# Kernel optimization log

Hardware: AMD Instinct MI355X
Metric: run time of the kernel (lower is better)

The kernel has to match this reference:

```python
import jax, jax.numpy as jnp
import numpy as np

B, D, T = 8, 1024, 512
HID, NH, NL = 256, 4, 2
OUT = HID // NH  # 64 per-head dim
ALPHA = 0.2      # leaky relu slope
EPS = 1e-5       # layernorm eps


def setup_inputs() -> dict:
    key = jax.random.key(0)
    ks = jax.random.split(key, 10)
    X_obs = jax.random.normal(ks[0], (B, D, T), dtype=jnp.float32)
    mask = (jax.random.uniform(ks[1], (B, D, T)) < 0.8).astype(jnp.float32)
    W_in = jax.random.normal(ks[2], (2 * T, HID), dtype=jnp.float32) * (1.0 / np.sqrt(2 * T))
    b_in = jnp.zeros((HID,), dtype=jnp.float32)
    gat_W = jax.random.normal(ks[3], (NL, NH, HID, OUT), dtype=jnp.float32) * (1.0 / np.sqrt(HID))
    gat_a = jax.random.normal(ks[4], (NL, NH, 2 * OUT), dtype=jnp.float32) * 0.1
    ln_g = jnp.ones((NL, HID), dtype=jnp.float32)
    ln_b = jnp.zeros((NL, HID), dtype=jnp.float32)
    W_out = jax.random.normal(ks[5], (HID, T), dtype=jnp.float32) * (1.0 / np.sqrt(HID))
    b_out = jnp.zeros((T,), dtype=jnp.float32)
    return dict(X_obs=X_obs, mask=mask, W_in=W_in, b_in=b_in, gat_W=gat_W,
                gat_a=gat_a, ln_g=ln_g, ln_b=ln_b, W_out=W_out, b_out=b_out)


def _layer_norm(x, g, b):
    mu = jnp.mean(x, axis=-1, keepdims=True)
    var = jnp.mean((x - mu) ** 2, axis=-1, keepdims=True)
    return (x - mu) * jax.lax.rsqrt(var + EPS) * g + b


def _gat_forward(X_obs, mask, W_in, b_in, gat_W, gat_a, ln_g, ln_b, W_out, b_out):
    # mean-impute per (d, t) position across batch
    obs_sum = jnp.sum(X_obs * mask, axis=0, keepdims=True)
    obs_cnt = jnp.sum(mask, axis=0, keepdims=True)
    pos_mean = obs_sum / (obs_cnt + 1e-10)
    X_mean = X_obs * mask + (1.0 - mask) * pos_mean

    x = jnp.concatenate([X_mean, mask], axis=-1)       # (B, D, 2T)
    h = x @ W_in + b_in                                 # (B, N, HID)

    for l in range(NL):
        Wl = gat_W[l]                                   # (H, HID, OUT)
        a_left = gat_a[l, :, :OUT]                      # (H, OUT)
        a_right = gat_a[l, :, OUT:]                     # (H, OUT)
        hW = jnp.einsum('bnd,hde->bhne', h, Wl)         # (B, H, N, OUT)
        # e_ij = leakyrelu(a_left . h_i + a_right . h_j) -- avoids O(N^2 * 2d) concat
        s_l = jnp.einsum('bhne,he->bhn', hW, a_left)
        s_r = jnp.einsum('bhne,he->bhn', hW, a_right)
        e = jax.nn.leaky_relu(s_l[..., :, None] + s_r[..., None, :], ALPHA)  # (B,H,N,N)
        attn = jax.nn.softmax(e, axis=-1)
        head_out = jnp.einsum('bhnm,bhme->bhne', attn, hW)                   # (B,H,N,OUT)
        h_new = jnp.transpose(head_out, (0, 2, 1, 3)).reshape(h.shape[0], h.shape[1], HID)
        h = _layer_norm(h + h_new, ln_g[l], ln_b[l])

    return h @ W_out + b_out                            # (B, D, T)


def reference(X_obs, mask, W_in, b_in, gat_W, gat_a, ln_g, ln_b, W_out, b_out):
    return _gat_forward(X_obs, mask, W_in, b_in, gat_W, gat_a, ln_g, ln_b, W_out, b_out)
```

## Files before the change

kernel.cpp:

```cpp
#include <hip/hip_runtime.h>
#include <hip/hip_bf16.h>

constexpr int B_   = 8;
constexpr int D_   = 1024;
constexpr int T_   = 512;
constexpr int HID_ = 256;
constexpr int NH_  = 4;
constexpr int NL_  = 2;
constexpr float ALPHA_ = 0.2f;
constexpr float EPS_   = 1e-5f;
constexpr int OUT_ = 64;
constexpr int M_ = B_ * D_;
constexpr int DT_ = D_ * T_;
constexpr int KIN_ = 2 * T_;

typedef __attribute__((ext_vector_type(8))) short short8;
typedef __attribute__((ext_vector_type(4))) float floatx4;

__device__ __forceinline__ unsigned short f2bf(float f) {
    unsigned int u = __float_as_uint(f);
    unsigned int r = u + 0x7fffu + ((u >> 16) & 1u);
    return (unsigned short)(r >> 16);
}
__device__ __forceinline__ unsigned int kenc(float f) {
    unsigned int u = __float_as_uint(f);
    return (u & 0x80000000u) ? ~u : (u | 0x80000000u);
}
__device__ __forceinline__ float kdec(unsigned int k) {
    unsigned int u = (k & 0x80000000u) ? (k ^ 0x80000000u) : ~k;
    return __uint_as_float(u);
}

__global__ __launch_bounds__(256) void prep_k(const float* __restrict__ X,
                                              const float* __restrict__ Mk,
                                              const float* __restrict__ W_in,
                                              const float* __restrict__ gatW,
                                              const float* __restrict__ W_out,
                                              unsigned short* __restrict__ Ain,
                                              unsigned short* __restrict__ Wt_in,
                                              unsigned short* __restrict__ Wcat,
                                              unsigned short* __restrict__ WtO,
                                              unsigned int* __restrict__ rmaxkey) {
    int bx = blockIdx.x;
    if (bx < 512) {
        int idx4 = (bx * 256 + threadIdx.x) * 4;
        int t = idx4 & (T_ - 1);
        int d = idx4 >> 9;
        float4 x[B_], m[B_];
        float4 s = {0, 0, 0, 0}, c = {0, 0, 0, 0};
#pragma unroll
        for (int b = 0; b < B_; b++) {
            x[b] = *(const float4*)&X[(size_t)b * DT_ + idx4];
            m[b] = *(const float4*)&Mk[(size_t)b * DT_ + idx4];
            s.x += x[b].x * m[b].x; s.y += x[b].y * m[b].y;
            s.z += x[b].z * m[b].z; s.w += x[b].w * m[b].w;
            c.x += m[b].x; c.y += m[b].y; c.z += m[b].z; c.w += m[b].w;
        }
        float4 pm;
        pm.x = s.x / (c.x + 1e-10f); pm.y = s.y / (c.y + 1e-10f);
        pm.z = s.z / (c.z + 1e-10f); pm.w = s.w / (c.w + 1e-10f);
#pragma unroll
        for (int b = 0; b < B_; b++) {
            size_t row = (size_t)b * D_ + d;
            ushort4 xm, mk;
            xm.x = f2bf(x[b].x * m[b].x + (1.f - m[b].x) * pm.x);
            xm.y = f2bf(x[b].y * m[b].y + (1.f - m[b].y) * pm.y);
            xm.z = f2bf(x[b].z * m[b].z + (1.f - m[b].z) * pm.z);
            xm.w = f2bf(x[b].w * m[b].w + (1.f - m[b].w) * pm.w);
            mk.x = f2bf(m[b].x); mk.y = f2bf(m[b].y);
            mk.z = f2bf(m[b].z); mk.w = f2bf(m[b].w);
            *(ushort4*)&Ain[row * KIN_ + t]      = xm;
            *(ushort4*)&Ain[row * KIN_ + T_ + t] = mk;
        }
    } else {
        int idx = (bx - 512) * 256 + threadIdx.x;
        if (idx < 64) rmaxkey[idx] = 0u;
        if (idx < 262144) {
            int n = idx >> 10, k = idx & 1023;
            Wt_in[idx] = f2bf(W_in[(size_t)k * HID_ + n]);
        } else if (idx < 393216) {
            int j = idx - 262144;
            int l = j >> 16, n = (j >> 8) & 255, k = j & 255;
            int h = n >> 6, e = n & 63;
            Wcat[j] = f2bf(gatW[(((size_t)(l * NH_ + h) * HID_) + k) * OUT_ + e]);
        } else {
            int j = idx - 393216;
            int n = j >> 8, k = j & 255;
            WtO[j] = f2bf(W_out[(size_t)k * T_ + n]);
        }
    }
}

template <int MODE>
__global__ __launch_bounds__(256) void gemm_bf16_k(
        const unsigned short* __restrict__ A,
        const unsigned short* __restrict__ Bt,
        const float* __restrict__ bias,
        float* __restrict__ C,
        unsigned short* __restrict__ Cb,
        const float* __restrict__ ga,
        float* __restrict__ s_l,
        float* __restrict__ s_r,
        unsigned int* __restrict__ rmaxkey,
        int Nsz, int Ksz) {
    __shared__ __align__(16) unsigned short As[2][64 * 72];
    __shared__ __align__(16) unsigned short Bs[2][64 * 72];
    int tid = threadIdx.x;
    int wave = tid >> 6, lane = tid & 63;
    int q = lane >> 4, r16 = lane & 15;
    int rowbase = blockIdx.y * 64;
    int colbase = blockIdx.x * 64;

    int srow = tid >> 3, sk = (tid & 7) * 8;
    const unsigned short* Ap0 = A + (size_t)(rowbase + srow) * Ksz + sk;
    const unsigned short* Ap1 = A + (size_t)(rowbase + srow + 32) * Ksz + sk;
    const unsigned short* Bp0 = Bt + (size_t)(colbase + srow) * Ksz + sk;
    const unsigned short* Bp1 = Bt + (size_t)(colbase + srow + 32) * Ksz + sk;
    int la0 = srow * 72 + sk, la1 = (srow + 32) * 72 + sk;

    floatx4 acc[4];
#pragma unroll
    for (int i = 0; i < 4; i++) acc[i] = (floatx4)0.f;

    uint4 pa0 = *(const uint4*)Ap0, pa1 = *(const uint4*)Ap1;
    uint4 pb0 = *(const uint4*)Bp0, pb1 = *(const uint4*)Bp1;
    *(uint4*)&As[0][la0] = pa0;
    *(uint4*)&As[0][la1] = pa1;
    *(uint4*)&Bs[0][la0] = pb0;
    *(uint4*)&Bs[0][la1] = pb1;

    int nk = Ksz >> 6;
    for (int it = 0; it < nk; it++) {
        int cur = it & 1;
        __syncthreads();
        if (it + 1 < nk) {
            int kt = (it + 1) << 6;
            pa0 = *(const uint4*)(Ap0 + kt);
            pa1 = *(const uint4*)(Ap1 + kt);
            pb0 = *(const uint4*)(Bp0 + kt);
            pb1 = *(const uint4*)(Bp1 + kt);
        }
#pragma unroll
        for (int t = 0; t < 2; t++) {
            short8 a = *(const short8*)&As[cur][(wave * 16 + r16) * 72 + t * 32 + q * 8];
#pragma unroll
            for (int ni = 0; ni < 4; ni++) {
                short8 b = *(const short8*)&Bs[cur][(ni * 16 + r16) * 72 + t * 32 + q * 8];
                acc[ni] = __builtin_amdgcn_mfma_f32_16x16x32_bf16(a, b, acc[ni], 0, 0, 0);
            }
        }
        if (it + 1 < nk) {
            int nxt = cur ^ 1;
            *(uint4*)&As[nxt][la0] = pa0;
            *(uint4*)&As[nxt][la1] = pa1;
            *(uint4*)&Bs[nxt][la0] = pb0;
            *(uint4*)&Bs[nxt][la1] = pb1;
        }
    }
    if constexpr (MODE == 2) {
        int bhh = ((rowbase >> 10) << 2) + blockIdx.x;
        int nb = (rowbase & (D_ - 1)) + wave * 16;
#pragma unroll
        for (int ni = 0; ni < 4; ni++) {
            int e = ni * 16 + r16;
            ushort4 pk;
            pk.x = f2bf(acc[ni][0]);
            pk.y = f2bf(acc[ni][1]);
            pk.z = f2bf(acc[ni][2]);
            pk.w = f2bf(acc[ni][3]);
            *(ushort4*)&Cb[((size_t)(bhh * 64 + e) << 10) + nb + q * 4] = pk;
        }
        const float* gab = ga + blockIdx.x * 2 * OUT_;
        float al4[4], ar4[4];
#pragma unroll
        for (int ni = 0; ni < 4; ni++) {
            al4[ni] = gab[ni * 16 + r16];
            ar4[ni] = gab[OUT_ + ni * 16 + r16];
        }
        float slv[4], srv[4];
#pragma unroll
        for (int rr = 0; rr < 4; rr++) {
            float s1 = 0.f, s2 = 0.f;
#pragma unroll
            for (int ni = 0; ni < 4; ni++) {
                s1 += acc[ni][rr] * al4[ni];
                s2 += acc[ni][rr] * ar4[ni];
            }
            slv[rr] = s1;
            srv[rr] = s2;
        }
#pragma unroll
        for (int off = 1; off < 16; off <<= 1) {
#pragma unroll
            for (int rr = 0; rr < 4; rr++) {
                slv[rr] += __shfl_xor(slv[rr], off, 64);
                srv[rr] += __shfl_xor(srv[rr], off, 64);
            }
        }
        {
            int rsel = r16 & 3;
            float sv = (rsel == 0) ? slv[0] : (rsel == 1) ? slv[1] : (rsel == 2) ? slv[2] : slv[3];
            float rv = (rsel == 0) ? srv[0] : (rsel == 1) ? srv[1] : (rsel == 2) ? srv[2] : srv[3];
            int n = nb + q * 4 + rsel;
            if (r16 < 4)                 s_l[bhh * D_ + n] = sv;
            else if (r16 >= 8 && r16 < 12) s_r[bhh * D_ + n] = rv;
        }
        float mx = fmaxf(fmaxf(srv[0], srv[1]), fmaxf(srv[2], srv[3]));
        mx = fmaxf(mx, __shfl_xor(mx, 16, 64));
        mx = fmaxf(mx, __shfl_xor(mx, 32, 64));
        if (lane == 0) atomicMax(&rmaxkey[bhh], kenc(mx));
    } else {
#pragma unroll
        for (int rr = 0; rr < 4; rr++) {
            int row = rowbase + wave * 16 + q * 4 + rr;
#pragma unroll
            for (int ni = 0; ni < 4; ni++) {
                int col = colbase + ni * 16 + r16;
                float v = acc[ni][rr] + (bias ? bias[col] : 0.f);
                C[(size_t)row * Nsz + col] = v;
                if constexpr (MODE == 1) Cb[(size_t)row * Nsz + col] = f2bf(v);
            }
        }
    }
}

__global__ __launch_bounds__(256) void attn_k(const unsigned short* __restrict__ hwT,
                                              const float* __restrict__ sl_g,
                                              const float* __restrict__ sr_g,
                                              const unsigned int* __restrict__ rmaxkey,
                                              float* __restrict__ pacc,
                                              float* __restrict__ pden) {
    int bh = blockIdx.x;
    int b = bh >> 2, h = bh & 3;
    int half = blockIdx.z;
    int mb = half * 512;
    int tid = threadIdx.x;
    int wave = tid >> 6, lane = tid & 63;
    int q = lane >> 4, r16 = lane & 15;

    __shared__ float srs[512];
    __shared__ __align__(16) unsigned short Vt[2][64][136];

    *(float2*)&srs[tid * 2] = *(const float2*)&sr_g[bh * D_ + mb + tid * 2];

    float rm = kdec(rmaxkey[bh]);
    int row0 = blockIdx.y * 64 + wave * 16;
    float sl = sl_g[bh * D_ + row0 + r16];
    float xm = sl + rm;
    float Mn = fmaxf(xm, ALPHA_ * xm);

    floatx4 acc[4];
#pragma unroll
    for (int i = 0; i < 4; i++) acc[i] = (floatx4)0.f;
    float dsum = 0.f;

    const unsigned short* vbase = hwT + ((size_t)(bh * 64) << 10) + mb;
    int se[4], sp[4];
#pragma unroll
    for (int i = 0; i < 4; i++) {
        int s = tid + i * 256;
        se[i] = s >> 4;
        sp[i] = (s & 15) * 8;
    }

    uint4 pre[4];
#pragma unroll
    for (int i = 0; i < 4; i++)
        pre[i] = *(const uint4*)&vbase[((size_t)se[i] << 10) + sp[i]];
#pragma unroll
    for (int i = 0; i < 4; i++)
        *(uint4*)&Vt[0][se[i]][sp[i]] = pre[i];
    __syncthreads();

    for (int c = 0; c < 4; c++) {
        int cur = c & 1;
        if (c < 3) {
            int mo = (c + 1) * 128;
#pragma unroll
            for (int i = 0; i < 4; i++)
                pre[i] = *(const uint4*)&vbase[((size_t)se[i] << 10) + mo + sp[i]];
        }
#pragma unroll
        for (int kk = 0; kk < 128; kk += 32) {
            int m0 = c * 128 + kk + q * 8;
            float4 s0 = *(const float4*)&srs[m0];
            float4 s1 = *(const float4*)&srs[m0 + 4];
            float sr8[8] = {s0.x, s0.y, s0.z, s0.w, s1.x, s1.y, s1.z, s1.w};
            float p[8];
#pragma unroll
            for (int j = 0; j < 8; j++) {
                float x = sl + sr8[j];
                float e = fmaxf(x, ALPHA_ * x);
                float pj = __expf(e - Mn);
                dsum += pj;
                p[j] = pj;
            }
            union { unsigned int u[4]; short8 s8; } cv;
#pragma unroll
            for (int j = 0; j < 4; j++) {
                unsigned int lo = (__float_as_uint(p[2 * j]) + 0x8000u) >> 16;
                unsigned int hi = (__float_as_uint(p[2 * j + 1]) + 0x8000u) & 0xffff0000u;
                cv.u[j] = hi | lo;
            }
#pragma unroll
            for (int ni = 0; ni < 4; ni++) {
                short8 bfr = *(const short8*)&Vt[cur][ni * 16 + r16][kk + q * 8];
                acc[ni] = __builtin_amdgcn_mfma_f32_16x16x32_bf16(cv.s8, bfr, acc[ni], 0, 0, 0);
            }
        }
        if (c < 3) {
#pragma unroll
            for (int i = 0; i < 4; i++)
                *(uint4*)&Vt[cur ^ 1][se[i]][sp[i]] = pre[i];
        }
        __syncthreads();
    }
    dsum += __shfl_xor(dsum, 16);
    dsum += __shfl_xor(dsum, 32);
    size_t gr0 = (size_t)b * D_ + row0;
    if (lane < 16) pden[((size_t)half * M_ + gr0 + r16) * NH_ + h] = dsum;
#pragma unroll
    for (int rr = 0; rr < 4; rr++) {
        size_t grow = gr0 + q * 4 + rr;
#pragma unroll
        for (int ni = 0; ni < 4; ni++) {
            pacc[((size_t)half * M_ + grow) * HID_ + h * OUT_ + ni * 16 + r16] = acc[ni][rr];
        }
    }
}

__global__ __launch_bounds__(256) void addln_k(float* __restrict__ h,
                                               const float* __restrict__ pacc,
                                               const float* __restrict__ pden,
                                               const float* __restrict__ g,
                                               const float* __restrict__ bb,
                                               unsigned short* __restrict__ hbf) {
    int wave = threadIdx.x >> 6, lane = threadIdx.x & 63;
    size_t row = (size_t)blockIdx.x * 4 + wave;
    float4 a  = *(const float4*)&h[row * HID_ + lane * 4];
    float4 p0 = *(const float4*)&pacc[row * HID_ + lane * 4];
    float4 p1 = *(const float4*)&pacc[((size_t)M_ + row) * HID_ + lane * 4];
    int hh = lane >> 4;
    float den = pden[row * NH_ + hh] + pden[((size_t)M_ + row) * NH_ + hh];
    float inv = 1.f / den;
    float4 v = {a.x + (p0.x + p1.x) * inv, a.y + (p0.y + p1.y) * inv,
                a.z + (p0.z + p1.z) * inv, a.w + (p0.w + p1.w) * inv};
    float s = v.x + v.y + v.z + v.w;
#pragma unroll
    for (int off = 1; off < 64; off <<= 1) s += __shfl_xor(s, off, 64);
    float mu = s * (1.f / HID_);
    float4 d = {v.x - mu, v.y - mu, v.z - mu, v.w - mu};
    float s2 = d.x * d.x + d.y * d.y + d.z * d.z + d.w * d.w;
#pragma unroll
    for (int off = 1; off < 64; off <<= 1) s2 += __shfl_xor(s2, off, 64);
    float rs = rsqrtf(s2 * (1.f / HID_) + EPS_);
    float4 gg = *(const float4*)&g[lane * 4];
    float4 bbv = *(const float4*)&bb[lane * 4];
    float4 res;
    res.x = d.x * rs * gg.x + bbv.x;
    res.y = d.y * rs * gg.y + bbv.y;
    res.z = d.z * rs * gg.z + bbv.z;
    res.w = d.w * rs * gg.w + bbv.w;
    *(float4*)&h[row * HID_ + lane * 4] = res;
    ushort4 pk = {f2bf(res.x), f2bf(res.y), f2bf(res.z), f2bf(res.w)};
    *(ushort4*)&hbf[row * HID_ + lane * 4] = pk;
}

extern "C" void kernel_launch(void* const* d_in, const int* in_sizes, int n_in,
                              void* d_out, int out_size, void* d_ws, size_t ws_size,
                              hipStream_t stream) {
    const float* X_obs = (const float*)d_in[0];
    const float* mask  = (const float*)d_in[1];
    const float* W_in  = (const float*)d_in[2];
    const float* b_in  = (const float*)d_in[3];
    const float* gat_W = (const float*)d_in[4];
    const float* gat_a = (const float*)d_in[5];
    const float* ln_g  = (const float*)d_in[6];
    const float* ln_b  = (const float*)d_in[7];
    const float* W_out = (const float*)d_in[8];
    const float* b_out = (const float*)d_in[9];
    float* out = (float*)d_out;

    char* base = (char*)d_ws;
    unsigned short* Ain  = (unsigned short*)base;
    unsigned short* hwT  = (unsigned short*)base;
    float* pacc = (float*)(base + (4u << 20));
    float* pden = (float*)(base + (20u << 20));
    float* hbuf = (float*)(base + (21u << 20));
    unsigned short* hbf   = (unsigned short*)(base + (29u << 20));
    unsigned short* Wt_in = (unsigned short*)(base + (33u << 20));
    unsigned short* Wcat  = Wt_in + (size_t)HID_ * KIN_;
    unsigned short* WtO   = Wcat + (size_t)NL_ * HID_ * HID_;
    float* slb = (float*)(WtO + (size_t)T_ * HID_);
    float* srb = slb + B_ * NH_ * D_;
    unsigned int* rmaxkey = (unsigned int*)(srb + B_ * NH_ * D_);

    prep_k<<<2560, 256, 0, stream>>>(X_obs, mask, W_in, gat_W, W_out,
                                     Ain, Wt_in, Wcat, WtO, rmaxkey);

    gemm_bf16_k<1><<<dim3(HID_ / 64, M_ / 64), 256, 0, stream>>>(
        Ain, Wt_in, b_in, hbuf, hbf, nullptr, nullptr, nullptr, nullptr,
        HID_, KIN_);

    for (int l = 0; l < NL_; l++) {
        gemm_bf16_k<2><<<dim3(HID_ / 64, M_ / 64), 256, 0, stream>>>(
            hbf, Wcat + (size_t)l * HID_ * HID_, nullptr, nullptr, hwT,
            gat_a + (size_t)l * NH_ * 2 * OUT_, slb, srb, rmaxkey + l * 32,
            HID_, HID_);
        attn_k<<<dim3(B_ * NH_, D_ / 64, 2), 256, 0, stream>>>(
            hwT, slb, srb, rmaxkey + l * 32, pacc, pden);
        addln_k<<<M_ / 4, 256, 0, stream>>>(hbuf, pacc, pden,
                                            ln_g + (size_t)l * HID_,
                                            ln_b + (size_t)l * HID_, hbf);
    }

    gemm_bf16_k<0><<<dim3(T_ / 64, M_ / 64), 256, 0, stream>>>(
        hbf, WtO, b_out, out, nullptr, nullptr, nullptr, nullptr, nullptr,
        T_, HID_);
}
```

Before: 217.0 us.

## Fuse residual layernorm into following GEMM and drop attention key-split

The separate add+layernorm kernel is removed. Its work is now done in a prologue of the next projection GEMM, which normalizes its 64-row A tile in shared memory. The attention kernel no longer splits the key dimension into two halves: each block walks all 1024 keys and writes normalized head outputs directly, so the partial accumulator and denominator buffers go away. In exchange, the layernorm is recomputed by every column block of the GEMM (4 or 8 times), and the attention grid halves, giving fewer blocks to fill the GPU.

```diff
diff --git a/kernel.cpp b/kernel.cpp
--- a/kernel.cpp
+++ b/kernel.cpp
@@ -228,20 +228,17 @@
                                               const float* __restrict__ sl_g,
                                               const float* __restrict__ sr_g,
                                               const unsigned int* __restrict__ rmaxkey,
-                                              float* __restrict__ pacc,
-                                              float* __restrict__ pden) {
+                                              float* __restrict__ hnew) {
     int bh = blockIdx.x;
     int b = bh >> 2, h = bh & 3;
-    int half = blockIdx.z;
-    int mb = half * 512;
     int tid = threadIdx.x;
     int wave = tid >> 6, lane = tid & 63;
     int q = lane >> 4, r16 = lane & 15;
 
-    __shared__ float srs[512];
+    __shared__ float srs[1024];
     __shared__ __align__(16) unsigned short Vt[2][64][136];
 
-    *(float2*)&srs[tid * 2] = *(const float2*)&sr_g[bh * D_ + mb + tid * 2];
+    *(float4*)&srs[tid * 4] = *(const float4*)&sr_g[bh * D_ + tid * 4];
 
     float rm = kdec(rmaxkey[bh]);
     int row0 = blockIdx.y * 64 + wave * 16;
@@ -254,7 +251,7 @@
     for (int i = 0; i < 4; i++) acc[i] = (floatx4)0.f;
     float dsum = 0.f;
 
-    const unsigned short* vbase = hwT + ((size_t)(bh * 64) << 10) + mb;
+    const unsigned short* vbase = hwT + ((size_t)(bh * 64) << 10);
     int se[4], sp[4];
 #pragma unroll
     for (int i = 0; i < 4; i++) {
@@ -272,9 +269,9 @@
         *(uint4*)&Vt[0][se[i]][sp[i]] = pre[i];
     __syncthreads();
 
-    for (int c = 0; c < 4; c++) {
+    for (int c = 0; c < 8; c++) {
         int cur = c & 1;
-        if (c < 3) {
+        if (c < 7) {
             int mo = (c + 1) * 128;
 #pragma unroll
             for (int i = 0; i < 4; i++)
@@ -308,7 +305,7 @@
                 acc[ni] = __builtin_amdgcn_mfma_f32_16x16x32_bf16(cv.s8, bfr, acc[ni], 0, 0, 0);
             }
         }
-        if (c < 3) {
+        if (c < 7) {
 #pragma unroll
             for (int i = 0; i < 4; i++)
                 *(uint4*)&Vt[cur ^ 1][se[i]][sp[i]] = pre[i];
@@ -317,53 +314,168 @@
     }
     dsum += __shfl_xor(dsum, 16);
     dsum += __shfl_xor(dsum, 32);
-    size_t gr0 = (size_t)b * D_ + row0;
-    if (lane < 16) pden[((size_t)half * M_ + gr0 + r16) * NH_ + h] = dsum;
 #pragma unroll
     for (int rr = 0; rr < 4; rr++) {
-        size_t grow = gr0 + q * 4 + rr;
+        float inv = 1.f / __shfl(dsum, q * 4 + rr, 64);
+        size_t off = ((size_t)(b * D_ + row0 + q * 4 + rr)) * HID_ + h * OUT_;
+#pragma unroll
+        for (int ni = 0; ni < 4; ni++)
+            hnew[off + ni * 16 + r16] = acc[ni][rr] * inv;
+    }
+}
+
+template <int MODE>
+__global__ __launch_bounds__(256) void gemmln_k(
+        const float* __restrict__ hbase,
+        const float* __restrict__ hnewIn,
+        const float* __restrict__ lng,
+        const float* __restrict__ lnb,
+        float* __restrict__ hout,
+        const unsigned short* __restrict__ Bt,
+        const float* __restrict__ bias,
+        float* __restrict__ C,
+        unsigned short* __restrict__ Cb,
+        const float* __restrict__ ga,
+        float* __restrict__ s_l,
+        float* __restrict__ s_r,
+        unsigned int* __restrict__ rmaxkey,
+        int Nsz) {
+    __shared__ __align__(16) unsigned short Asf[64 * 264];
+    __shared__ __align__(16) unsigned short Bs[2][64 * 72];
+    int tid = threadIdx.x;
+    int wave = tid >> 6, lane = tid & 63;
+    int q = lane >> 4, r16 = lane & 15;
+    int rowbase = blockIdx.y * 64;
+    int colbase = blockIdx.x * 64;
+
+    {
+        float4 gg = *(const float4*)&lng[lane * 4];
+        float4 bv = *(const float4*)&lnb[lane * 4];
+        for (int rr = 0; rr < 16; ++rr) {
+            int row = wave * 16 + rr;
+            size_t grow = (size_t)(rowbase + row) * HID_ + lane * 4;
+            float4 a  = *(const float4*)&hbase[grow];
+            float4 nv = *(const float4*)&hnewIn[grow];
+            float4 v = {a.x + nv.x, a.y + nv.y, a.z + nv.z, a.w + nv.w};
+            float s = v.x + v.y + v.z + v.w;
+#pragma unroll
+            for (int off = 1; off < 64; off <<= 1) s += __shfl_xor(s, off, 64);
+            float mu = s * (1.f / HID_);
+            float4 dd = {v.x - mu, v.y - mu, v.z - mu, v.w - mu};
+            float s2 = dd.x * dd.x + dd.y * dd.y + dd.z * dd.z + dd.w * dd.w;
+#pragma unroll
+            for (int off = 1; off < 64; off <<= 1) s2 += __shfl_xor(s2, off, 64);
+            float rs = rsqrtf(s2 * (1.f / HID_) + EPS_);
+            float4 res;
+            res.x = dd.x * rs * gg.x + bv.x;
+            res.y = dd.y * rs * gg.y + bv.y;
+            res.z = dd.z * rs * gg.z + bv.z;
+            res.w = dd.w * rs * gg.w + bv.w;
+            if (hout && blockIdx.x == 0) *(float4*)&hout[grow] = res;
+            ushort4 pk = {f2bf(res.x), f2bf(res.y), f2bf(res.z), f2bf(res.w)};
+            *(ushort4*)&Asf[row * 264 + lane * 4] = pk;
+        }
+    }
+    int srow = tid >> 3, sk = (tid & 7) * 8;
+    const unsigned short* Bp0 = Bt + (size_t)(colbase + srow) * HID_ + sk;
+    const unsigned short* Bp1 = Bt + (size_t)(colbase + srow + 32) * HID_ + sk;
+    int la0 = srow * 72 + sk, la1 = (srow + 32) * 72 + sk;
+    uint4 pb0 = *(const uint4*)Bp0, pb1 = *(const uint4*)Bp1;
+    *(uint4*)&Bs[0][la0] = pb0;
+    *(uint4*)&Bs[0][la1] = pb1;
+    __syncthreads();
+
+    floatx4 acc[4];
+#pragma unroll
+    for (int i = 0; i < 4; i++) acc[i] = (floatx4)0.f;
+
+    constexpr int nk = HID_ / 64;
+    for (int it = 0; it < nk; it++) {
+        int cur = it & 1;
+        if (it + 1 < nk) {
+            int kt = (it + 1) << 6;
+            pb0 = *(const uint4*)(Bp0 + kt);
+            pb1 = *(const uint4*)(Bp1 + kt);
+        }
+#pragma unroll
+        for (int t = 0; t < 2; t++) {
+            short8 a = *(const short8*)&Asf[(wave * 16 + r16) * 264 + it * 64 + t * 32 + q * 8];
+#pragma unroll
+            for (int ni = 0; ni < 4; ni++) {
+                short8 b = *(const short8*)&Bs[cur][(ni * 16 + r16) * 72 + t * 32 + q * 8];
+                acc[ni] = __builtin_amdgcn_mfma_f32_16x16x32_bf16(a, b, acc[ni], 0, 0, 0);
+            }
+        }
+        if (it + 1 < nk) {
+            int nxt = cur ^ 1;
+            *(uint4*)&Bs[nxt][la0] = pb0;
+            *(uint4*)&Bs[nxt][la1] = pb1;
+        }
+        __syncthreads();
+    }
+    if constexpr (MODE == 2) {
+        int bhh = ((rowbase >> 10) << 2) + blockIdx.x;
+        int nb = (rowbase & (D_ - 1)) + wave * 16;
 #pragma unroll
         for (int ni = 0; ni < 4; ni++) {
-            pacc[((size_t)half * M_ + grow) * HID_ + h * OUT_ + ni * 16 + r16] = acc[ni][rr];
-        }
-    }
-}
-
-__global__ __launch_bounds__(256) void addln_k(float* __restrict__ h,
-                                               const float* __restrict__ pacc,
-                                               const float* __restrict__ pden,
-                                               const float* __restrict__ g,
-                                               const float* __restrict__ bb,
-                                               unsigned short* __restrict__ hbf) {
-    int wave = threadIdx.x >> 6, lane = threadIdx.x & 63;
-    size_t row = (size_t)blockIdx.x * 4 + wave;
-    float4 a  = *(const float4*)&h[row * HID_ + lane * 4];
-    float4 p0 = *(const float4*)&pacc[row * HID_ + lane * 4];
-    float4 p1 = *(const float4*)&pacc[((size_t)M_ + row) * HID_ + lane * 4];
-    int hh = lane >> 4;
-    float den = pden[row * NH_ + hh] + pden[((size_t)M_ + row) * NH_ + hh];
-    float inv = 1.f / den;
-    float4 v = {a.x + (p0.x + p1.x) * inv, a.y + (p0.y + p1.y) * inv,
-                a.z + (p0.z + p1.z) * inv, a.w + (p0.w + p1.w) * inv};
-    float s = v.x + v.y + v.z + v.w;
-#pragma unroll
-    for (int off = 1; off < 64; off <<= 1) s += __shfl_xor(s, off, 64);
-    float mu = s * (1.f / HID_);
-    float4 d = {v.x - mu, v.y - mu, v.z - mu, v.w - mu};
-    float s2 = d.x * d.x + d.y * d.y + d.z * d.z + d.w * d.w;
-#pragma unroll
-    for (int off = 1; off < 64; off <<= 1) s2 += __shfl_xor(s2, off, 64);
-    float rs = rsqrtf(s2 * (1.f / HID_) + EPS_);
-    float4 gg = *(const float4*)&g[lane * 4];
-    float4 bbv = *(const float4*)&bb[lane * 4];
-    float4 res;
-    res.x = d.x * rs * gg.x + bbv.x;
-    res.y = d.y * rs * gg.y + bbv.y;
-    res.z = d.z * rs * gg.z + bbv.z;
-    res.w = d.w * rs * gg.w + bbv.w;
-    *(float4*)&h[row * HID_ + lane * 4] = res;
-    ushort4 pk = {f2bf(res.x), f2bf(res.y), f2bf(res.z), f2bf(res.w)};
-    *(ushort4*)&hbf[row * HID_ + lane * 4] = pk;
+            int e = ni * 16 + r16;
+            ushort4 pk;
+            pk.x = f2bf(acc[ni][0]);
+            pk.y = f2bf(acc[ni][1]);
+            pk.z = f2bf(acc[ni][2]);
+            pk.w = f2bf(acc[ni][3]);
+            *(ushort4*)&Cb[((size_t)(bhh * 64 + e) << 10) + nb + q * 4] = pk;
+        }
+        const float* gab = ga + blockIdx.x * 2 * OUT_;
+        float al4[4], ar4[4];
+#pragma unroll
+        for (int ni = 0; ni < 4; ni++) {
+            al4[ni] = gab[ni * 16 + r16];
+            ar4[ni] = gab[OUT_ + ni * 16 + r16];
+        }
+        float slv[4], srv[4];
+#pragma unroll
+        for (int rr = 0; rr < 4; rr++) {
+            float s1 = 0.f, s2 = 0.f;
+#pragma unroll
+            for (int ni = 0; ni < 4; ni++) {
+                s1 += acc[ni][rr] * al4[ni];
+                s2 += acc[ni][rr] * ar4[ni];
+            }
+            slv[rr] = s1;
+            srv[rr] = s2;
+        }
+#pragma unroll
+        for (int off = 1; off < 16; off <<= 1) {
+#pragma unroll
+            for (int rr = 0; rr < 4; rr++) {
+                slv[rr] += __shfl_xor(slv[rr], off, 64);
+                srv[rr] += __shfl_xor(srv[rr], off, 64);
+            }
+        }
+        {
+            int rsel = r16 & 3;
+            float sv = (rsel == 0) ? slv[0] : (rsel == 1) ? slv[1] : (rsel == 2) ? slv[2] : slv[3];
+            float rv = (rsel == 0) ? srv[0] : (rsel == 1) ? srv[1] : (rsel == 2) ? srv[2] : srv[3];
+            int n = nb + q * 4 + rsel;
+            if (r16 < 4)                 s_l[bhh * D_ + n] = sv;
+            else if (r16 >= 8 && r16 < 12) s_r[bhh * D_ + n] = rv;
+        }
+        float mx = fmaxf(fmaxf(srv[0], srv[1]), fmaxf(srv[2], srv[3]));
+        mx = fmaxf(mx, __shfl_xor(mx, 16, 64));
+        mx = fmaxf(mx, __shfl_xor(mx, 32, 64));
+        if (lane == 0) atomicMax(&rmaxkey[bhh], kenc(mx));
+    } else {
+#pragma unroll
+        for (int rr = 0; rr < 4; rr++) {
+            int row = rowbase + wave * 16 + q * 4 + rr;
+#pragma unroll
+            for (int ni = 0; ni < 4; ni++) {
+                int col = colbase + ni * 16 + r16;
+                C[(size_t)row * Nsz + col] = acc[ni][rr] + bias[col];
+            }
+        }
+    }
 }
 
 extern "C" void kernel_launch(void* const* d_in, const int* in_sizes, int n_in,
@@ -384,11 +496,12 @@
     char* base = (char*)d_ws;
     unsigned short* Ain  = (unsigned short*)base;
     unsigned short* hwT  = (unsigned short*)base;
-    float* pacc = (float*)(base + (4u << 20));
-    float* pden = (float*)(base + (20u << 20));
-    float* hbuf = (float*)(base + (21u << 20));
+    float* hnew0 = (float*)(base + (4u << 20));
+    float* hnew1 = (float*)(base + (12u << 20));
+    float* hbufA = (float*)(base + (21u << 20));
     unsigned short* hbf   = (unsigned short*)(base + (29u << 20));
-    unsigned short* Wt_in = (unsigned short*)(base + (33u << 20));
+    float* hbufB = (float*)(base + (33u << 20));
+    unsigned short* Wt_in = (unsigned short*)(base + (42u << 20));
     unsigned short* Wcat  = Wt_in + (size_t)HID_ * KIN_;
     unsigned short* WtO   = Wcat + (size_t)NL_ * HID_ * HID_;
     float* slb = (float*)(WtO + (size_t)T_ * HID_);
@@ -399,22 +512,24 @@
                                      Ain, Wt_in, Wcat, WtO, rmaxkey);
 
     gemm_bf16_k<1><<<dim3(HID_ / 64, M_ / 64), 256, 0, stream>>>(
-        Ain, Wt_in, b_in, hbuf, hbf, nullptr, nullptr, nullptr, nullptr,
+        Ain, Wt_in, b_in, hbufA, hbf, nullptr, nullptr, nullptr, nullptr,
         HID_, KIN_);
 
-    for (int l = 0; l < NL_; l++) {
-        gemm_bf16_k<2><<<dim3(HID_ / 64, M_ / 64), 256, 0, stream>>>(
-            hbf, Wcat + (size_t)l * HID_ * HID_, nullptr, nullptr, hwT,
-            gat_a + (size_t)l * NH_ * 2 * OUT_, slb, srb, rmaxkey + l * 32,
-            HID_, HID_);
-        attn_k<<<dim3(B_ * NH_, D_ / 64, 2), 256, 0, stream>>>(
-            hwT, slb, srb, rmaxkey + l * 32, pacc, pden);
-        addln_k<<<M_ / 4, 256, 0, stream>>>(hbuf, pacc, pden,
-                                            ln_g + (size_t)l * HID_,
-                                            ln_b + (size_t)l * HID_, hbf);
-    }
-
-    gemm_bf16_k<0><<<dim3(T_ / 64, M_ / 64), 256, 0, stream>>>(
-        hbf, WtO, b_out, out, nullptr, nullptr, nullptr, nullptr, nullptr,
-        T_, HID_);
-}
+    gemm_bf16_k<2><<<dim3(HID_ / 64, M_ / 64), 256, 0, stream>>>(
+        hbf, Wcat, nullptr, nullptr, hwT,
+        gat_a, slb, srb, rmaxkey, HID_, HID_);
+    attn_k<<<dim3(B_ * NH_, D_ / 64), 256, 0, stream>>>(
+        hwT, slb, srb, rmaxkey, hnew0);
+
+    gemmln_k<2><<<dim3(HID_ / 64, M_ / 64), 256, 0, stream>>>(
+        hbufA, hnew0, ln_g, ln_b, hbufB,
+        Wcat + (size_t)HID_ * HID_, nullptr, nullptr, hwT,
+        gat_a + (size_t)NH_ * 2 * OUT_, slb, srb, rmaxkey + 32, HID_);
+    attn_k<<<dim3(B_ * NH_, D_ / 64), 256, 0, stream>>>(
+        hwT, slb, srb, rmaxkey + 32, hnew1);
+
+    gemmln_k<0><<<dim3(T_ / 64, M_ / 64), 256, 0, stream>>>(
+        hbufB, hnew1, ln_g + HID_, ln_b + HID_, nullptr,
+        WtO, b_out, out, nullptr,
+        nullptr, nullptr, nullptr, nullptr, T_);
+}
```

Result: slower. 243.7 us (+12.3%).

## Split attention over output-feature halves instead of key halves, normalize in-kernel

Applied to the files above, without the earlier changes.

The attention kernel now gives each block all 1024 keys but only 32 of the 64 head-output features, rather than splitting the keys into two halves. This removes the two partial accumulator/denominator buffers and the cross-half reduction in the add+layernorm kernel, since each block can normalize its own output. The trade-off is that the exp/softmax weights are computed twice, once per feature half, and each block runs twice as many MFMA iterations over fewer columns. Exponentials also switch to exp2f with inputs prescaled by log2(e).

```diff
diff --git a/kernel.cpp b/kernel.cpp
--- a/kernel.cpp
+++ b/kernel.cpp
@@ -228,56 +228,59 @@
                                               const float* __restrict__ sl_g,
                                               const float* __restrict__ sr_g,
                                               const unsigned int* __restrict__ rmaxkey,
-                                              float* __restrict__ pacc,
-                                              float* __restrict__ pden) {
+                                              float* __restrict__ hnew) {
     int bh = blockIdx.x;
     int b = bh >> 2, h = bh & 3;
-    int half = blockIdx.z;
-    int mb = half * 512;
+    int eh = blockIdx.z;
     int tid = threadIdx.x;
     int wave = tid >> 6, lane = tid & 63;
     int q = lane >> 4, r16 = lane & 15;
 
-    __shared__ float srs[512];
-    __shared__ __align__(16) unsigned short Vt[2][64][136];
-
-    *(float2*)&srs[tid * 2] = *(const float2*)&sr_g[bh * D_ + mb + tid * 2];
-
-    float rm = kdec(rmaxkey[bh]);
+    __shared__ float srs[1024];
+    __shared__ __align__(16) unsigned short Vt[2][32][136];
+
+    constexpr float L2E = 1.4426950408889634f;
+    {
+        float4 v = *(const float4*)&sr_g[bh * D_ + tid * 4];
+        v.x *= L2E; v.y *= L2E; v.z *= L2E; v.w *= L2E;
+        *(float4*)&srs[tid * 4] = v;
+    }
+
+    float rm = kdec(rmaxkey[bh]) * L2E;
     int row0 = blockIdx.y * 64 + wave * 16;
-    float sl = sl_g[bh * D_ + row0 + r16];
+    float sl = sl_g[bh * D_ + row0 + r16] * L2E;
     float xm = sl + rm;
     float Mn = fmaxf(xm, ALPHA_ * xm);
 
-    floatx4 acc[4];
-#pragma unroll
-    for (int i = 0; i < 4; i++) acc[i] = (floatx4)0.f;
+    floatx4 acc[2];
+    acc[0] = (floatx4)0.f;
+    acc[1] = (floatx4)0.f;
     float dsum = 0.f;
 
-    const unsigned short* vbase = hwT + ((size_t)(bh * 64) << 10) + mb;
-    int se[4], sp[4];
-#pragma unroll
-    for (int i = 0; i < 4; i++) {
+    const unsigned short* vbase = hwT + ((size_t)(bh * 64 + eh * 32) << 10);
+    int se[2], sp[2];
+#pragma unroll
+    for (int i = 0; i < 2; i++) {
         int s = tid + i * 256;
         se[i] = s >> 4;
         sp[i] = (s & 15) * 8;
     }
 
-    uint4 pre[4];
-#pragma unroll
-    for (int i = 0; i < 4; i++)
+    uint4 pre[2];
+#pragma unroll
+    for (int i = 0; i < 2; i++)
         pre[i] = *(const uint4*)&vbase[((size_t)se[i] << 10) + sp[i]];
 #pragma unroll
-    for (int i = 0; i < 4; i++)
+    for (int i = 0; i < 2; i++)
         *(uint4*)&Vt[0][se[i]][sp[i]] = pre[i];
     __syncthreads();
 
-    for (int c = 0; c < 4; c++) {
+    for (int c = 0; c < 8; c++) {
         int cur = c & 1;
-        if (c < 3) {
+        if (c < 7) {
             int mo = (c + 1) * 128;
 #pragma unroll
-            for (int i = 0; i < 4; i++)
+            for (int i = 0; i < 2; i++)
                 pre[i] = *(const uint4*)&vbase[((size_t)se[i] << 10) + mo + sp[i]];
         }
 #pragma unroll
@@ -291,7 +294,7 @@
             for (int j = 0; j < 8; j++) {
                 float x = sl + sr8[j];
                 float e = fmaxf(x, ALPHA_ * x);
-                float pj = __expf(e - Mn);
+                float pj = exp2f(e - Mn);
                 dsum += pj;
                 p[j] = pj;
             }
@@ -303,48 +306,40 @@
                 cv.u[j] = hi | lo;
             }
 #pragma unroll
-            for (int ni = 0; ni < 4; ni++) {
+            for (int ni = 0; ni < 2; ni++) {
                 short8 bfr = *(const short8*)&Vt[cur][ni * 16 + r16][kk + q * 8];
                 acc[ni] = __builtin_amdgcn_mfma_f32_16x16x32_bf16(cv.s8, bfr, acc[ni], 0, 0, 0);
             }
         }
-        if (c < 3) {
-#pragma unroll
-            for (int i = 0; i < 4; i++)
+        if (c < 7) {
+#pragma unroll
+            for (int i = 0; i < 2; i++)
                 *(uint4*)&Vt[cur ^ 1][se[i]][sp[i]] = pre[i];
         }
         __syncthreads();
     }
     dsum += __shfl_xor(dsum, 16);
     dsum += __shfl_xor(dsum, 32);
-    size_t gr0 = (size_t)b * D_ + row0;
-    if (lane < 16) pden[((size_t)half * M_ + gr0 + r16) * NH_ + h] = dsum;
 #pragma unroll
     for (int rr = 0; rr < 4; rr++) {
-        size_t grow = gr0 + q * 4 + rr;
-#pragma unroll
-        for (int ni = 0; ni < 4; ni++) {
-            pacc[((size_t)half * M_ + grow) * HID_ + h * OUT_ + ni * 16 + r16] = acc[ni][rr];
-        }
+        float inv = 1.f / __shfl(dsum, q * 4 + rr, 64);
+        size_t off = ((size_t)(b * D_ + row0 + q * 4 + rr)) * HID_ + h * OUT_ + eh * 32;
+#pragma unroll
+        for (int ni = 0; ni < 2; ni++)
+            hnew[off + ni * 16 + r16] = acc[ni][rr] * inv;
     }
 }
 
 __global__ __launch_bounds__(256) void addln_k(float* __restrict__ h,
-                                               const float* __restrict__ pacc,
-                                               const float* __restrict__ pden,
+                                               const float* __restrict__ hnew,
                                                const float* __restrict__ g,
                                                const float* __restrict__ bb,
                                                unsigned short* __restrict__ hbf) {
     int wave = threadIdx.x >> 6, lane = threadIdx.x & 63;
     size_t row = (size_t)blockIdx.x * 4 + wave;
     float4 a  = *(const float4*)&h[row * HID_ + lane * 4];
-    float4 p0 = *(const float4*)&pacc[row * HID_ + lane * 4];
-    float4 p1 = *(const float4*)&pacc[((size_t)M_ + row) * HID_ + lane * 4];
-    int hh = lane >> 4;
-    float den = pden[row * NH_ + hh] + pden[((size_t)M_ + row) * NH_ + hh];
-    float inv = 1.f / den;
-    float4 v = {a.x + (p0.x + p1.x) * inv, a.y + (p0.y + p1.y) * inv,
-                a.z + (p0.z + p1.z) * inv, a.w + (p0.w + p1.w) * inv};
+    float4 nv = *(const float4*)&hnew[row * HID_ + lane * 4];
+    float4 v = {a.x + nv.x, a.y + nv.y, a.z + nv.z, a.w + nv.w};
     float s = v.x + v.y + v.z + v.w;
 #pragma unroll
     for (int off = 1; off < 64; off <<= 1) s += __shfl_xor(s, off, 64);
@@ -384,8 +379,7 @@
     char* base = (char*)d_ws;
     unsigned short* Ain  = (unsigned short*)base;
     unsigned short* hwT  = (unsigned short*)base;
-    float* pacc = (float*)(base + (4u << 20));
-    float* pden = (float*)(base + (20u << 20));
+    float* hnew = (float*)(base + (4u << 20));
     float* hbuf = (float*)(base + (21u << 20));
     unsigned short* hbf   = (unsigned short*)(base + (29u << 20));
     unsigned short* Wt_in = (unsigned short*)(base + (33u << 20));
@@ -408,8 +402,8 @@
             gat_a + (size_t)l * NH_ * 2 * OUT_, slb, srb, rmaxkey + l * 32,
             HID_, HID_);
         attn_k<<<dim3(B_ * NH_, D_ / 64, 2), 256, 0, stream>>>(
-            hwT, slb, srb, rmaxkey + l * 32, pacc, pden);
-        addln_k<<<M_ / 4, 256, 0, stream>>>(hbuf, pacc, pden,
+            hwT, slb, srb, rmaxkey + l * 32, hnew);
+        addln_k<<<M_ / 4, 256, 0, stream>>>(hbuf, hnew,
                                             ln_g + (size_t)l * HID_,
                                             ln_b + (size_t)l * HID_, hbf);
     }
```

New measurement: 237.2 us. +9.3%, slower.
